# Performance work log

Hardware: AMD Instinct MI355X
Metric: run time of the kernel (lower is better)

## Reference

```python
import jax, jax.numpy as jnp
import numpy as np

N = 100000   # num nodes
D = 64       # in_channels == out_channels (forced by zeros_like(x) accumulator)
E = 400000   # edges per edge type
T = 5        # number of edge types (hardcoded list in the module)


def setup_inputs() -> dict:
    key = jax.random.key(0)
    k1, k2, k3, k4, k5 = jax.random.split(key, 5)
    x = jax.random.normal(k1, (N, D), dtype=jnp.float32)
    # 5 edge types, each [2, E] of node indices (row 0 = src, row 1 = dst)
    edges = jax.random.randint(k2, (T, 2, E), 0, N)
    # per-edge-type Linear(2D -> D): weight [2D, D] and bias [D]
    W = jax.random.normal(k3, (T, 2 * D, D), dtype=jnp.float32) * (1.0 / np.sqrt(2 * D))
    b = jax.random.normal(k4, (T, D), dtype=jnp.float32) * 0.01
    edge_attention = jax.random.normal(k5, (T,), dtype=jnp.float32)
    return {"x": x, "W": W, "b": b, "edge_attention": edge_attention, "edges": edges}


def reference(x, W, b, edge_attention, edges):
    # softmax over the 5 edge types (F.softmax(self.edge_attention, dim=0))
    weights = jax.nn.softmax(edge_attention)              # [T]
    src = edges[:, 0, :]                                  # [T, E]
    dst = edges[:, 1, :]                                  # [T, E]
    # gather: edge_features = cat([x[src], x[dst]], dim=1)
    feats = jnp.concatenate([x[src], x[dst]], axis=-1)    # [T, E, 2D]
    # per-edge-type MLP: Linear(2D->D) + ReLU
    proj = jax.nn.relu(jnp.einsum('tef,tfd->ted', feats, W) + b[:, None, :])  # [T, E, D]
    # scatter-add into src nodes, then mean via clamped bincount
    seg_sum = jax.vmap(lambda s, p: jax.ops.segment_sum(p, s, num_segments=N))(src, proj)  # [T, N, D]
    counts = jax.vmap(lambda s: jax.ops.segment_sum(jnp.ones(s.shape, jnp.float32), s, num_segments=N))(src)  # [T, N]
    counts = jnp.maximum(counts, 1.0)[:, :, None]         # clamp(min=1)
    node_proj = seg_sum / counts                          # [T, N, D]
    # attention-weighted sum across edge types
    return jnp.einsum('t,tnd->nd', weights, node_proj)    # [N, D]
```

## Files before the change

### kernel.cpp

```cpp
#include <hip/hip_runtime.h>
#include <hip/hip_bf16.h>

#define NN 100000
#define DD 64
#define EE 400000
#define TT 5

#define CH 16
#define BPC 6250
#define PSPLIT 32
#define PESL (EE / PSPLIT)
#define PBN (TT * CH * PSPLIT)
#define PB_IDX(t, c, s) ((((t) * CH + (c)) * PSPLIT) + (s))

#define SCAN_TOTAL 500000
#define SCAN_T 256
#define SCAN_PER 1024
#define SCAN_B 512

typedef __bf16 bf16x8 __attribute__((ext_vector_type(8)));
typedef float  f32x4  __attribute__((ext_vector_type(4)));

#define OFF_XBF  0u
#define OFF_WT   12800000u
#define OFF_CTOT 12881920u
#define OFF_WGT  14881920u
#define OFF_CUR  14881984u
#define OFF_BS   16881984u
#define OFF_BO   16884032u
#define OFF_PE   16886080u
#define OFF_PB   24886080u
#define OFF_DST  24914240u
#define OFF_SEG  32914240u

__device__ __forceinline__ unsigned short f2bf(float f) {
    union { float f; unsigned u; } v; v.f = f;
    unsigned u = v.u;
    return (unsigned short)((u + 0x7FFFu + ((u >> 16) & 1u)) >> 16);
}

__global__ void k_init(const float* __restrict__ x, const float* __restrict__ W,
                       const float* __restrict__ ea,
                       unsigned short* __restrict__ xbf, unsigned short* __restrict__ wT,
                       float* __restrict__ wgt, float* __restrict__ out) {
    int i = blockIdx.x * blockDim.x + threadIdx.x;
    if (i < NN * DD) {
        out[i] = 0.0f;
        xbf[i] = f2bf(x[i]);
    }
    if (i < TT * 128 * 64) {
        int t = i >> 13;
        int rem = i & 8191;
        int d = rem >> 7;
        int k = rem & 127;
        wT[i] = f2bf(W[t * 8192 + k * 64 + d]);
    }
    if (i == 0) {
        float m = -1e30f;
        for (int t = 0; t < TT; t++) m = fmaxf(m, ea[t]);
        float e[TT]; float s = 0.0f;
        for (int t = 0; t < TT; t++) { e[t] = __expf(ea[t] - m); s += e[t]; }
        for (int t = 0; t < TT; t++) wgt[t] = e[t] / s;
    }
}

__global__ __launch_bounds__(256) void k_pcount(const int* __restrict__ edges,
                                                unsigned* __restrict__ pcnt) {
    const int s = blockIdx.x, t = blockIdx.y;
    __shared__ unsigned h[CH];
    if (threadIdx.x < CH) h[threadIdx.x] = 0u;
    __syncthreads();
    const int4* srcp = reinterpret_cast<const int4*>(edges + (size_t)t * 2 * EE + s * PESL);
    for (int i = threadIdx.x; i < PESL / 4; i += 256) {
        int4 v = srcp[i];
        atomicAdd(&h[(unsigned)v.x / BPC], 1u);
        atomicAdd(&h[(unsigned)v.y / BPC], 1u);
        atomicAdd(&h[(unsigned)v.z / BPC], 1u);
        atomicAdd(&h[(unsigned)v.w / BPC], 1u);
    }
    __syncthreads();
    if (threadIdx.x < CH) pcnt[PB_IDX(t, threadIdx.x, s)] = h[threadIdx.x];
}

__global__ void k_pscan(unsigned* __restrict__ pb) {
    __shared__ unsigned s[256];
    const int tid = threadIdx.x;
    unsigned v[10]; unsigned sum = 0u;
#pragma unroll
    for (int j = 0; j < 10; j++) { v[j] = pb[tid * 10 + j]; sum += v[j]; }
    s[tid] = sum;
    __syncthreads();
    unsigned inc = sum;
    for (int d = 1; d < 256; d <<= 1) {
        unsigned a = (tid >= d) ? s[tid - d] : 0u;
        __syncthreads();
        inc += a;
        s[tid] = inc;
        __syncthreads();
    }
    unsigned run = inc - sum;
#pragma unroll
    for (int j = 0; j < 10; j++) { unsigned c = v[j]; pb[tid * 10 + j] = run; run += c; }
    if (tid == 255) pb[PBN] = run;
}

__global__ __launch_bounds__(256) void k_pscat(const int* __restrict__ edges,
                                               const unsigned* __restrict__ pbase,
                                               unsigned* __restrict__ pe) {
    const int s = blockIdx.x, t = blockIdx.y;
    __shared__ unsigned lofs[CH];
    if (threadIdx.x < CH) lofs[threadIdx.x] = pbase[PB_IDX(t, threadIdx.x, s)];
    __syncthreads();
    const int* srcp = edges + (size_t)t * 2 * EE + s * PESL;
    const int* dstp = srcp + EE;
    for (int i = threadIdx.x; i < PESL / 4; i += 256) {
        int4 v = reinterpret_cast<const int4*>(srcp)[i];
        int4 w = reinterpret_cast<const int4*>(dstp)[i];
        {
            unsigned c = (unsigned)v.x / BPC;
            unsigned o = atomicAdd(&lofs[c], 1u);
            pe[o] = (((unsigned)v.x - c * BPC) << 17) | (unsigned)w.x;
        }
        {
            unsigned c = (unsigned)v.y / BPC;
            unsigned o = atomicAdd(&lofs[c], 1u);
            pe[o] = (((unsigned)v.y - c * BPC) << 17) | (unsigned)w.y;
        }
        {
            unsigned c = (unsigned)v.z / BPC;
            unsigned o = atomicAdd(&lofs[c], 1u);
            pe[o] = (((unsigned)v.z - c * BPC) << 17) | (unsigned)w.z;
        }
        {
            unsigned c = (unsigned)v.w / BPC;
            unsigned o = atomicAdd(&lofs[c], 1u);
            pe[o] = (((unsigned)v.w - c * BPC) << 17) | (unsigned)w.w;
        }
    }
}

__global__ __launch_bounds__(512) void k_bcount(const unsigned* __restrict__ pe,
                                                const unsigned* __restrict__ pbase,
                                                unsigned* __restrict__ cnt_tot) {
    const int c = blockIdx.x, t = blockIdx.y;
    __shared__ unsigned h[BPC];
    for (int i = threadIdx.x; i < BPC; i += 512) h[i] = 0u;
    __syncthreads();
    const unsigned st = pbase[PB_IDX(t, c, 0)];
    const unsigned en = pbase[((t * CH + c) + 1) * PSPLIT];
    for (unsigned i = st + threadIdx.x; i < en; i += 512)
        atomicAdd(&h[pe[i] >> 17], 1u);
    __syncthreads();
    unsigned* outp = cnt_tot + t * NN + c * BPC;
    for (int i = threadIdx.x; i < BPC; i += 512) outp[i] = h[i];
}

__global__ void k_scan1(const unsigned* __restrict__ cnt_tot,
                        unsigned* __restrict__ cur, unsigned* __restrict__ bsum) {
    __shared__ unsigned s[SCAN_T];
    const int b = blockIdx.x, tid = threadIdx.x;
    const int base = b * SCAN_PER + tid * 4;
    unsigned tot[4] = {0u, 0u, 0u, 0u};
    if (base < SCAN_TOTAL) {
        uint4 tv = *reinterpret_cast<const uint4*>(cnt_tot + base);
        tot[0] = tv.x; tot[1] = tv.y; tot[2] = tv.z; tot[3] = tv.w;
    }
    const unsigned tsum = tot[0] + tot[1] + tot[2] + tot[3];
    s[tid] = tsum;
    __syncthreads();
    unsigned inc = tsum;
    for (int d = 1; d < SCAN_T; d <<= 1) {
        unsigned add = (tid >= d) ? s[tid - d] : 0u;
        __syncthreads();
        inc += add;
        s[tid] = inc;
        __syncthreads();
    }
    if (tid == SCAN_T - 1) bsum[b] = inc;
    const unsigned p0 = inc - tsum;
    if (base < SCAN_TOTAL) {
        *reinterpret_cast<uint4*>(cur + base) =
            make_uint4(p0, p0 + tot[0], p0 + tot[0] + tot[1], p0 + tot[0] + tot[1] + tot[2]);
    }
}

__global__ void k_scan2(const unsigned* __restrict__ bsum, unsigned* __restrict__ boff) {
    __shared__ unsigned s[SCAN_B];
    const int tid = threadIdx.x;
    const unsigned v = bsum[tid];
    s[tid] = v;
    __syncthreads();
    unsigned inc = v;
    for (int d = 1; d < SCAN_B; d <<= 1) {
        unsigned add = (tid >= d) ? s[tid - d] : 0u;
        __syncthreads();
        inc += add;
        s[tid] = inc;
        __syncthreads();
    }
    boff[tid] = inc - v;
}

__global__ __launch_bounds__(512) void k_bfill(const unsigned* __restrict__ pe,
                                               const unsigned* __restrict__ pbase,
                                               const unsigned* __restrict__ cur,
                                               const unsigned* __restrict__ boff,
                                               const unsigned* __restrict__ cnt_tot,
                                               int* __restrict__ sdst,
                                               int* __restrict__ seg) {
    const int c = blockIdx.x, t = blockIdx.y;
    __shared__ unsigned curl[BPC];
    const int n0 = c * BPC;
    for (int i = threadIdx.x; i < BPC; i += 512) {
        int g = t * NN + n0 + i;
        unsigned start = cur[g] + boff[g >> 10];
        curl[i] = start;
        unsigned cc = cnt_tot[g];
        int node = n0 + i;
        for (unsigned j = 0; j < cc; j++) seg[start + j] = node;
    }
    __syncthreads();
    const unsigned st = pbase[PB_IDX(t, c, 0)];
    const unsigned en = pbase[((t * CH + c) + 1) * PSPLIT];
    for (unsigned i = st + threadIdx.x; i < en; i += 512) {
        unsigned p = pe[i];
        sdst[atomicAdd(&curl[p >> 17], 1u)] = (int)(p & 0x1FFFFu);
    }
}

__global__ __launch_bounds__(256) void k_edge(
    const unsigned short* __restrict__ xbf, const unsigned short* __restrict__ wT,
    const float* __restrict__ b, const int* __restrict__ sdst,
    const int* __restrict__ seg, const unsigned* __restrict__ cnt,
    const float* __restrict__ wgt, float* __restrict__ out) {
    const int t  = blockIdx.y;
    const int e0 = blockIdx.x * 128;

    __shared__ __align__(16) unsigned short Ab[128][136];
    __shared__ float scale_s[128];
    __shared__ int   src_s[132];

    const int tid = threadIdx.x;

    {
        int e = tid >> 1, half = tid & 1;
        size_t pos = (size_t)t * EE + e0 + e;
        int idx = half ? sdst[pos] : seg[pos];
        const float4* g = reinterpret_cast<const float4*>(xbf + (size_t)idx * 64);
        float4* l = reinterpret_cast<float4*>(&Ab[e][half * 64]);
#pragma unroll
        for (int c = 0; c < 8; c++) l[c] = g[c];
        if (half == 0) {
            src_s[e] = idx;
            scale_s[e] = wgt[t] / (float)cnt[t * NN + idx];
        }
    }
    __syncthreads();

    const int wv = tid >> 6, lane = tid & 63;
    const int m16 = lane & 15, quad = lane >> 4;
    const unsigned short* wrow = wT + (size_t)t * 8192;

    f32x4 acc[2][4];
#pragma unroll
    for (int tm = 0; tm < 2; tm++)
#pragma unroll
        for (int tn = 0; tn < 4; tn++)
            acc[tm][tn] = (f32x4){0.f, 0.f, 0.f, 0.f};

#pragma unroll
    for (int kk = 0; kk < 128; kk += 32) {
        const int kb = kk + quad * 8;
        bf16x8 af[2], bfr[4];
#pragma unroll
        for (int tm = 0; tm < 2; tm++)
            af[tm] = *reinterpret_cast<const bf16x8*>(&Ab[wv * 32 + tm * 16 + m16][kb]);
#pragma unroll
        for (int tn = 0; tn < 4; tn++)
            bfr[tn] = *reinterpret_cast<const bf16x8*>(wrow + (tn * 16 + m16) * 128 + kb);
#pragma unroll
        for (int tm = 0; tm < 2; tm++)
#pragma unroll
            for (int tn = 0; tn < 4; tn++)
                acc[tm][tn] = __builtin_amdgcn_mfma_f32_16x16x32_bf16(
                    af[tm], bfr[tn], acc[tm][tn], 0, 0, 0);
    }

    __syncthreads();

    float bias[4];
#pragma unroll
    for (int tn = 0; tn < 4; tn++) bias[tn] = b[t * 64 + tn * 16 + m16];

    float* proj = reinterpret_cast<float*>(&Ab[0][0]);
#pragma unroll
    for (int tm = 0; tm < 2; tm++) {
#pragma unroll
        for (int r = 0; r < 4; r++) {
            const int eloc = wv * 32 + tm * 16 + quad * 4 + r;
            const float s = scale_s[eloc];
#pragma unroll
            for (int tn = 0; tn < 4; tn++) {
                float v = acc[tm][tn][r] + bias[tn];
                v = v > 0.f ? v : 0.f;
                proj[eloc * 68 + tn * 16 + m16] = v * s;
            }
        }
    }

    {
        const int j0 = wv * 32;
        float sum = 0.f;
#pragma unroll
        for (int j = j0; j < j0 + 32; j++) {
            sum += proj[j * 68 + lane];
            const bool flush = (j == j0 + 31) || (src_s[j + 1] != src_s[j]);
            if (flush) {
                atomicAdd(out + (size_t)src_s[j] * 64 + lane, sum);
                sum = 0.f;
            }
        }
    }
}

extern "C" void kernel_launch(void* const* d_in, const int* in_sizes, int n_in,
                              void* d_out, int out_size, void* d_ws, size_t ws_size,
                              hipStream_t stream) {
    const float* x     = (const float*)d_in[0];
    const float* W     = (const float*)d_in[1];
    const float* b     = (const float*)d_in[2];
    const float* ea    = (const float*)d_in[3];
    const int*   edges = (const int*)d_in[4];
    float* out = (float*)d_out;

    char* ws = (char*)d_ws;
    unsigned short* xbf  = (unsigned short*)(ws + OFF_XBF);
    unsigned short* wT   = (unsigned short*)(ws + OFF_WT);
    unsigned* cnt_tot    = (unsigned*)(ws + OFF_CTOT);
    float* wgt           = (float*)(ws + OFF_WGT);
    unsigned* cur        = (unsigned*)(ws + OFF_CUR);
    unsigned* bsum       = (unsigned*)(ws + OFF_BS);
    unsigned* boff       = (unsigned*)(ws + OFF_BO);
    unsigned* pe         = (unsigned*)(ws + OFF_PE);
    unsigned* pb         = (unsigned*)(ws + OFF_PB);
    int* sdst            = (int*)(ws + OFF_DST);
    int* seg             = (int*)(ws + OFF_SEG);

    k_init<<<(NN * DD) / 256, 256, 0, stream>>>(x, W, ea, xbf, wT, wgt, out);

    k_pcount<<<dim3(PSPLIT, TT), 256, 0, stream>>>(edges, pb);
    k_pscan<<<1, 256, 0, stream>>>(pb);
    k_pscat<<<dim3(PSPLIT, TT), 256, 0, stream>>>(edges, pb, pe);
    k_bcount<<<dim3(CH, TT), 512, 0, stream>>>(pe, pb, cnt_tot);
    k_scan1<<<SCAN_B, SCAN_T, 0, stream>>>(cnt_tot, cur, bsum);
    k_scan2<<<1, SCAN_B, 0, stream>>>(bsum, boff);
    k_bfill<<<dim3(CH, TT), 512, 0, stream>>>(pe, pb, cur, boff, cnt_tot, sdst, seg);

    dim3 grid(EE / 128, TT);
    k_edge<<<grid, 256, 0, stream>>>(xbf, wT, b, sdst, seg, cnt_tot, wgt, out);
}
```

Before: 339.8 us.

## Assign node ranges per block, accumulate in shared memory, drop global atomics

The edge kernel now launches one block per 64-node range instead of one per 128 edges of one type. Each block walks the CSR-sorted edges of all five types whose source falls in its range, in 32-edge chunks per wave. It accumulates results with LDS atomics and then writes the output rows directly. This removes the output zeroing in init and the global float atomics. In exchange there is load imbalance across blocks, per-chunk padding waste, and a per-wave loop with no block-level sync between the shared Ab/proj reuse steps.

```diff
diff --git a/kernel.cpp b/kernel.cpp
--- a/kernel.cpp
+++ b/kernel.cpp
@@ -17,6 +17,9 @@
 #define SCAN_T 256
 #define SCAN_PER 1024
 #define SCAN_B 512
+
+#define NB 64
+#define NBLK ((NN + NB - 1) / NB)
 
 typedef __bf16 bf16x8 __attribute__((ext_vector_type(8)));
 typedef float  f32x4  __attribute__((ext_vector_type(4)));
@@ -42,10 +45,9 @@
 __global__ void k_init(const float* __restrict__ x, const float* __restrict__ W,
                        const float* __restrict__ ea,
                        unsigned short* __restrict__ xbf, unsigned short* __restrict__ wT,
-                       float* __restrict__ wgt, float* __restrict__ out) {
+                       float* __restrict__ wgt) {
     int i = blockIdx.x * blockDim.x + threadIdx.x;
     if (i < NN * DD) {
-        out[i] = 0.0f;
         xbf[i] = f2bf(x[i]);
     }
     if (i < TT * 128 * 64) {
@@ -228,98 +230,149 @@
     }
 }
 
-__global__ __launch_bounds__(256) void k_edge(
+__global__ __launch_bounds__(256) void k_edge4(
     const unsigned short* __restrict__ xbf, const unsigned short* __restrict__ wT,
     const float* __restrict__ b, const int* __restrict__ sdst,
     const int* __restrict__ seg, const unsigned* __restrict__ cnt,
+    const unsigned* __restrict__ cur, const unsigned* __restrict__ boff,
     const float* __restrict__ wgt, float* __restrict__ out) {
-    const int t  = blockIdx.y;
-    const int e0 = blockIdx.x * 128;
+
+    const int n0 = blockIdx.x * NB;
+    const int n1 = (n0 + NB < NN) ? (n0 + NB) : NN;
+    const int tid = threadIdx.x;
+    const int wv = tid >> 6, lane = tid & 63;
+    const int m16 = lane & 15, quad = lane >> 4;
 
     __shared__ __align__(16) unsigned short Ab[128][136];
+    __shared__ __align__(16) float accs[NB][64];
     __shared__ float scale_s[128];
     __shared__ int   src_s[132];
 
-    const int tid = threadIdx.x;
-
     {
-        int e = tid >> 1, half = tid & 1;
-        size_t pos = (size_t)t * EE + e0 + e;
-        int idx = half ? sdst[pos] : seg[pos];
-        const float4* g = reinterpret_cast<const float4*>(xbf + (size_t)idx * 64);
-        float4* l = reinterpret_cast<float4*>(&Ab[e][half * 64]);
-#pragma unroll
-        for (int c = 0; c < 8; c++) l[c] = g[c];
-        if (half == 0) {
-            src_s[e] = idx;
-            scale_s[e] = wgt[t] / (float)cnt[t * NN + idx];
-        }
-    }
-    __syncthreads();
-
-    const int wv = tid >> 6, lane = tid & 63;
-    const int m16 = lane & 15, quad = lane >> 4;
-    const unsigned short* wrow = wT + (size_t)t * 8192;
-
-    f32x4 acc[2][4];
-#pragma unroll
-    for (int tm = 0; tm < 2; tm++)
-#pragma unroll
-        for (int tn = 0; tn < 4; tn++)
-            acc[tm][tn] = (f32x4){0.f, 0.f, 0.f, 0.f};
-
-#pragma unroll
-    for (int kk = 0; kk < 128; kk += 32) {
-        const int kb = kk + quad * 8;
-        bf16x8 af[2], bfr[4];
+        float4* a4 = reinterpret_cast<float4*>(&accs[0][0]);
+        for (int i = tid; i < NB * 16; i += 256) a4[i] = make_float4(0.f, 0.f, 0.f, 0.f);
+    }
+
+    unsigned p0t[TT], p1t[TT];
+    int nw[TT], NW = 0;
+#pragma unroll
+    for (int t = 0; t < TT; t++) {
+        int g0 = t * NN + n0;
+        int g1 = t * NN + n1;
+        unsigned p0 = cur[g0] + boff[g0 >> 10];
+        unsigned p1 = (g1 >= SCAN_TOTAL) ? (unsigned)(TT * EE)
+                                         : (cur[g1] + boff[g1 >> 10]);
+        p0t[t] = p0; p1t[t] = p1;
+        nw[t] = (int)((p1 - p0 + 31u) >> 5);
+        NW += nw[t];
+    }
+
+    __syncthreads();
+
+    for (int k = wv; k < NW; k += 4) {
+        int t = 0, rem = k;
+#pragma unroll
+        for (int tt = 0; tt < TT - 1; tt++)
+            if (t == tt && rem >= nw[tt]) { rem -= nw[tt]; t = tt + 1; }
+        unsigned p0s = p0t[0], p1s = p1t[0];
+#pragma unroll
+        for (int tt = 1; tt < TT; tt++)
+            if (t == tt) { p0s = p0t[tt]; p1s = p1t[tt]; }
+        const unsigned ts = p0s + ((unsigned)rem << 5);
+        const unsigned left = p1s - ts;
+        const int rows = (int)((left < 32u) ? left : 32u);
+        const float wgt_t = wgt[t];
+
+        {
+            const int e = lane >> 1, half = lane & 1;
+            const int r = wv * 32 + e;
+            float4* l = reinterpret_cast<float4*>(&Ab[r][half * 64]);
+            if (e < rows) {
+                const unsigned pos = ts + (unsigned)e;
+                const int idx = half ? sdst[pos] : seg[pos];
+                const float4* g = reinterpret_cast<const float4*>(xbf + (size_t)idx * 64);
+#pragma unroll
+                for (int cc = 0; cc < 8; cc++) l[cc] = g[cc];
+                if (half == 0) {
+                    src_s[r] = idx - n0;
+                    scale_s[r] = wgt_t / (float)cnt[t * NN + idx];
+                }
+            } else {
+                const float4 z = make_float4(0.f, 0.f, 0.f, 0.f);
+#pragma unroll
+                for (int cc = 0; cc < 8; cc++) l[cc] = z;
+                if (half == 0) { src_s[r] = 0; scale_s[r] = 0.f; }
+            }
+        }
+
+        const unsigned short* wrow = wT + (size_t)t * 8192;
+
+        f32x4 acc[2][4];
 #pragma unroll
         for (int tm = 0; tm < 2; tm++)
-            af[tm] = *reinterpret_cast<const bf16x8*>(&Ab[wv * 32 + tm * 16 + m16][kb]);
-#pragma unroll
-        for (int tn = 0; tn < 4; tn++)
-            bfr[tn] = *reinterpret_cast<const bf16x8*>(wrow + (tn * 16 + m16) * 128 + kb);
-#pragma unroll
-        for (int tm = 0; tm < 2; tm++)
 #pragma unroll
             for (int tn = 0; tn < 4; tn++)
-                acc[tm][tn] = __builtin_amdgcn_mfma_f32_16x16x32_bf16(
-                    af[tm], bfr[tn], acc[tm][tn], 0, 0, 0);
-    }
-
-    __syncthreads();
-
-    float bias[4];
-#pragma unroll
-    for (int tn = 0; tn < 4; tn++) bias[tn] = b[t * 64 + tn * 16 + m16];
-
-    float* proj = reinterpret_cast<float*>(&Ab[0][0]);
-#pragma unroll
-    for (int tm = 0; tm < 2; tm++) {
-#pragma unroll
-        for (int r = 0; r < 4; r++) {
-            const int eloc = wv * 32 + tm * 16 + quad * 4 + r;
-            const float s = scale_s[eloc];
-#pragma unroll
-            for (int tn = 0; tn < 4; tn++) {
-                float v = acc[tm][tn][r] + bias[tn];
-                v = v > 0.f ? v : 0.f;
-                proj[eloc * 68 + tn * 16 + m16] = v * s;
+                acc[tm][tn] = (f32x4){0.f, 0.f, 0.f, 0.f};
+
+#pragma unroll
+        for (int kk = 0; kk < 128; kk += 32) {
+            const int kb = kk + quad * 8;
+            bf16x8 af[2], bfr[4];
+#pragma unroll
+            for (int tm = 0; tm < 2; tm++)
+                af[tm] = *reinterpret_cast<const bf16x8*>(&Ab[wv * 32 + tm * 16 + m16][kb]);
+#pragma unroll
+            for (int tn = 0; tn < 4; tn++)
+                bfr[tn] = *reinterpret_cast<const bf16x8*>(wrow + (tn * 16 + m16) * 128 + kb);
+#pragma unroll
+            for (int tm = 0; tm < 2; tm++)
+#pragma unroll
+                for (int tn = 0; tn < 4; tn++)
+                    acc[tm][tn] = __builtin_amdgcn_mfma_f32_16x16x32_bf16(
+                        af[tm], bfr[tn], acc[tm][tn], 0, 0, 0);
+        }
+
+        float bias[4];
+#pragma unroll
+        for (int tn = 0; tn < 4; tn++) bias[tn] = b[t * 64 + tn * 16 + m16];
+
+        float* proj = reinterpret_cast<float*>(&Ab[0][0]);
+#pragma unroll
+        for (int tm = 0; tm < 2; tm++) {
+#pragma unroll
+            for (int r = 0; r < 4; r++) {
+                const int eloc = wv * 32 + tm * 16 + quad * 4 + r;
+                const float s = scale_s[eloc];
+#pragma unroll
+                for (int tn = 0; tn < 4; tn++) {
+                    float v = acc[tm][tn][r] + bias[tn];
+                    v = v > 0.f ? v : 0.f;
+                    proj[eloc * 68 + tn * 16 + m16] = v * s;
+                }
             }
         }
-    }
-
+
+        {
+            const int j0 = wv * 32;
+            float sum = 0.f;
+#pragma unroll
+            for (int j = j0; j < j0 + 32; j++) {
+                sum += proj[j * 68 + lane];
+                const bool flush = (j == j0 + 31) || (src_s[j + 1] != src_s[j]);
+                if (flush) {
+                    atomicAdd(&accs[src_s[j]][lane], sum);
+                    sum = 0.f;
+                }
+            }
+        }
+    }
+
+    __syncthreads();
     {
-        const int j0 = wv * 32;
-        float sum = 0.f;
-#pragma unroll
-        for (int j = j0; j < j0 + 32; j++) {
-            sum += proj[j * 68 + lane];
-            const bool flush = (j == j0 + 31) || (src_s[j + 1] != src_s[j]);
-            if (flush) {
-                atomicAdd(out + (size_t)src_s[j] * 64 + lane, sum);
-                sum = 0.f;
-            }
-        }
+        const int rows = n1 - n0;
+        const float4* a4 = reinterpret_cast<const float4*>(&accs[0][0]);
+        float4* o4 = reinterpret_cast<float4*>(out + (size_t)n0 * 64);
+        for (int i = tid; i < rows * 16; i += 256) o4[i] = a4[i];
     }
 }
 
@@ -346,7 +399,7 @@
     int* sdst            = (int*)(ws + OFF_DST);
     int* seg             = (int*)(ws + OFF_SEG);
 
-    k_init<<<(NN * DD) / 256, 256, 0, stream>>>(x, W, ea, xbf, wT, wgt, out);
+    k_init<<<(NN * DD) / 256, 256, 0, stream>>>(x, W, ea, xbf, wT, wgt);
 
     k_pcount<<<dim3(PSPLIT, TT), 256, 0, stream>>>(edges, pb);
     k_pscan<<<1, 256, 0, stream>>>(pb);
@@ -356,6 +409,6 @@
     k_scan2<<<1, SCAN_B, 0, stream>>>(bsum, boff);
     k_bfill<<<dim3(CH, TT), 512, 0, stream>>>(pe, pb, cur, boff, cnt_tot, sdst, seg);
 
-    dim3 grid(EE / 128, TT);
-    k_edge<<<grid, 256, 0, stream>>>(xbf, wT, b, sdst, seg, cnt_tot, wgt, out);
-}
+    k_edge4<<<NBLK, 256, 0, stream>>>(xbf, wT, b, sdst, seg, cnt_tot,
+                                      cur, boff, wgt, out);
+}
```

Result: slower. 486.8 us (+43.3%).

## Load MFMA A-fragments directly from global and raise bucket count to forty

Applied to the files above, without the earlier changes.

The edge kernel no longer stages gathered bf16 node rows in shared memory. Each wave now handles 16 edges and loads its A fragments straight from global memory into registers, with 64 edges per block and a higher occupancy bound. Separately, the bucketing pass uses 40 chunks of 2500 nodes instead of 16, giving the bucket-count and bucket-fill kernels more blocks, and the prefix scan is widened to 512 threads to match. In exchange, each weight fragment is reused over fewer edges, and the gather becomes strided global loads instead of coalesced row copies.

```diff
diff --git a/kernel.cpp b/kernel.cpp
--- a/kernel.cpp
+++ b/kernel.cpp
@@ -6,8 +6,8 @@
 #define EE 400000
 #define TT 5
 
-#define CH 16
-#define BPC 6250
+#define CH 40
+#define BPC 2500
 #define PSPLIT 32
 #define PESL (EE / PSPLIT)
 #define PBN (TT * CH * PSPLIT)
@@ -83,15 +83,19 @@
 }
 
 __global__ void k_pscan(unsigned* __restrict__ pb) {
-    __shared__ unsigned s[256];
+    __shared__ unsigned s[512];
     const int tid = threadIdx.x;
-    unsigned v[10]; unsigned sum = 0u;
-#pragma unroll
-    for (int j = 0; j < 10; j++) { v[j] = pb[tid * 10 + j]; sum += v[j]; }
+    unsigned v[13]; unsigned sum = 0u;
+#pragma unroll
+    for (int j = 0; j < 13; j++) {
+        int g = tid * 13 + j;
+        v[j] = (g < PBN) ? pb[g] : 0u;
+        sum += v[j];
+    }
     s[tid] = sum;
     __syncthreads();
     unsigned inc = sum;
-    for (int d = 1; d < 256; d <<= 1) {
+    for (int d = 1; d < 512; d <<= 1) {
         unsigned a = (tid >= d) ? s[tid - d] : 0u;
         __syncthreads();
         inc += a;
@@ -100,8 +104,12 @@
     }
     unsigned run = inc - sum;
 #pragma unroll
-    for (int j = 0; j < 10; j++) { unsigned c = v[j]; pb[tid * 10 + j] = run; run += c; }
-    if (tid == 255) pb[PBN] = run;
+    for (int j = 0; j < 13; j++) {
+        int g = tid * 13 + j;
+        if (g < PBN) pb[g] = run;
+        run += v[j];
+    }
+    if (tid == 511) pb[PBN] = run;
 }
 
 __global__ __launch_bounds__(256) void k_pscat(const int* __restrict__ edges,
@@ -228,93 +236,76 @@
     }
 }
 
-__global__ __launch_bounds__(256) void k_edge(
+__global__ __launch_bounds__(256, 8) void k_edge5(
     const unsigned short* __restrict__ xbf, const unsigned short* __restrict__ wT,
     const float* __restrict__ b, const int* __restrict__ sdst,
     const int* __restrict__ seg, const unsigned* __restrict__ cnt,
     const float* __restrict__ wgt, float* __restrict__ out) {
     const int t  = blockIdx.y;
-    const int e0 = blockIdx.x * 128;
-
-    __shared__ __align__(16) unsigned short Ab[128][136];
-    __shared__ float scale_s[128];
-    __shared__ int   src_s[132];
+    const int e0 = blockIdx.x * 64;
+
+    __shared__ __align__(16) float proj[64][68];
+    __shared__ float scale_s[64];
+    __shared__ int   src_s[68];
 
     const int tid = threadIdx.x;
-
-    {
-        int e = tid >> 1, half = tid & 1;
-        size_t pos = (size_t)t * EE + e0 + e;
-        int idx = half ? sdst[pos] : seg[pos];
-        const float4* g = reinterpret_cast<const float4*>(xbf + (size_t)idx * 64);
-        float4* l = reinterpret_cast<float4*>(&Ab[e][half * 64]);
-#pragma unroll
-        for (int c = 0; c < 8; c++) l[c] = g[c];
-        if (half == 0) {
-            src_s[e] = idx;
-            scale_s[e] = wgt[t] / (float)cnt[t * NN + idx];
-        }
-    }
-    __syncthreads();
-
     const int wv = tid >> 6, lane = tid & 63;
     const int m16 = lane & 15, quad = lane >> 4;
+    const int row = wv * 16 + m16;
+
+    const size_t pos = (size_t)t * EE + e0 + row;
+    const int srcI = seg[pos];
+    const int dstI = sdst[pos];
+    if (quad == 0) {
+        src_s[row] = srcI;
+        scale_s[row] = wgt[t] / (float)cnt[t * NN + srcI];
+    }
+
     const unsigned short* wrow = wT + (size_t)t * 8192;
-
-    f32x4 acc[2][4];
-#pragma unroll
-    for (int tm = 0; tm < 2; tm++)
-#pragma unroll
-        for (int tn = 0; tn < 4; tn++)
-            acc[tm][tn] = (f32x4){0.f, 0.f, 0.f, 0.f};
-
-#pragma unroll
-    for (int kk = 0; kk < 128; kk += 32) {
-        const int kb = kk + quad * 8;
-        bf16x8 af[2], bfr[4];
-#pragma unroll
-        for (int tm = 0; tm < 2; tm++)
-            af[tm] = *reinterpret_cast<const bf16x8*>(&Ab[wv * 32 + tm * 16 + m16][kb]);
+    const unsigned short* arow_s = xbf + (size_t)srcI * 64;
+    const unsigned short* arow_d = xbf + (size_t)dstI * 64;
+
+    f32x4 acc[4];
+#pragma unroll
+    for (int tn = 0; tn < 4; tn++) acc[tn] = (f32x4){0.f, 0.f, 0.f, 0.f};
+
+#pragma unroll
+    for (int k4 = 0; k4 < 4; k4++) {
+        const int off = (k4 & 1) * 32 + quad * 8;
+        const bf16x8 af = *reinterpret_cast<const bf16x8*>((k4 < 2 ? arow_s : arow_d) + off);
+        const int kb = k4 * 32 + quad * 8;
+        bf16x8 bfr[4];
 #pragma unroll
         for (int tn = 0; tn < 4; tn++)
             bfr[tn] = *reinterpret_cast<const bf16x8*>(wrow + (tn * 16 + m16) * 128 + kb);
 #pragma unroll
-        for (int tm = 0; tm < 2; tm++)
-#pragma unroll
-            for (int tn = 0; tn < 4; tn++)
-                acc[tm][tn] = __builtin_amdgcn_mfma_f32_16x16x32_bf16(
-                    af[tm], bfr[tn], acc[tm][tn], 0, 0, 0);
-    }
-
-    __syncthreads();
+        for (int tn = 0; tn < 4; tn++)
+            acc[tn] = __builtin_amdgcn_mfma_f32_16x16x32_bf16(af, bfr[tn], acc[tn], 0, 0, 0);
+    }
 
     float bias[4];
 #pragma unroll
     for (int tn = 0; tn < 4; tn++) bias[tn] = b[t * 64 + tn * 16 + m16];
 
-    float* proj = reinterpret_cast<float*>(&Ab[0][0]);
-#pragma unroll
-    for (int tm = 0; tm < 2; tm++) {
-#pragma unroll
-        for (int r = 0; r < 4; r++) {
-            const int eloc = wv * 32 + tm * 16 + quad * 4 + r;
-            const float s = scale_s[eloc];
-#pragma unroll
-            for (int tn = 0; tn < 4; tn++) {
-                float v = acc[tm][tn][r] + bias[tn];
-                v = v > 0.f ? v : 0.f;
-                proj[eloc * 68 + tn * 16 + m16] = v * s;
-            }
+#pragma unroll
+    for (int r = 0; r < 4; r++) {
+        const int eloc = wv * 16 + quad * 4 + r;
+        const float s = scale_s[eloc];
+#pragma unroll
+        for (int tn = 0; tn < 4; tn++) {
+            float v = acc[tn][r] + bias[tn];
+            v = v > 0.f ? v : 0.f;
+            proj[eloc][tn * 16 + m16] = v * s;
         }
     }
 
     {
-        const int j0 = wv * 32;
+        const int j0 = wv * 16;
         float sum = 0.f;
 #pragma unroll
-        for (int j = j0; j < j0 + 32; j++) {
-            sum += proj[j * 68 + lane];
-            const bool flush = (j == j0 + 31) || (src_s[j + 1] != src_s[j]);
+        for (int j = j0; j < j0 + 16; j++) {
+            sum += proj[j][lane];
+            const bool flush = (j == j0 + 15) || (src_s[j + 1] != src_s[j]);
             if (flush) {
                 atomicAdd(out + (size_t)src_s[j] * 64 + lane, sum);
                 sum = 0.f;
@@ -349,13 +340,13 @@
     k_init<<<(NN * DD) / 256, 256, 0, stream>>>(x, W, ea, xbf, wT, wgt, out);
 
     k_pcount<<<dim3(PSPLIT, TT), 256, 0, stream>>>(edges, pb);
-    k_pscan<<<1, 256, 0, stream>>>(pb);
+    k_pscan<<<1, 512, 0, stream>>>(pb);
     k_pscat<<<dim3(PSPLIT, TT), 256, 0, stream>>>(edges, pb, pe);
     k_bcount<<<dim3(CH, TT), 512, 0, stream>>>(pe, pb, cnt_tot);
     k_scan1<<<SCAN_B, SCAN_T, 0, stream>>>(cnt_tot, cur, bsum);
     k_scan2<<<1, SCAN_B, 0, stream>>>(bsum, boff);
     k_bfill<<<dim3(CH, TT), 512, 0, stream>>>(pe, pb, cur, boff, cnt_tot, sdst, seg);
 
-    dim3 grid(EE / 128, TT);
-    k_edge<<<grid, 256, 0, stream>>>(xbf, wT, b, sdst, seg, cnt_tot, wgt, out);
-}
+    dim3 grid(EE / 64, TT);
+    k_edge5<<<grid, 256, 0, stream>>>(xbf, wT, b, sdst, seg, cnt_tot, wgt, out);
+}
```

Result: slower. 418.7 us (+23.2%).

## Fuse partition count into init kernel and raise bucket count to forty

Applied to the files above, without the earlier changes.

Merges the per-slice partition histogram into the init kernel: its first 160 blocks also count source-node buckets, which removes one kernel launch. It also raises the coarse bucket count from 16 to 40 (2500 nodes each), so the bcount and bfill grids get more blocks and each block handles a smaller range. The partition scan now runs with 512 threads to cover the larger table. Risks: the new work makes the first 160 init blocks much longer than the rest, and the downstream kernels may have assumptions about bucket size, such as shared-memory sizing, that are not visible here.

```diff
diff --git a/kernel.cpp b/kernel.cpp
--- a/kernel.cpp
+++ b/kernel.cpp
@@ -6,8 +6,8 @@
 #define EE 400000
 #define TT 5
 
-#define CH 16
-#define BPC 6250
+#define CH 40
+#define BPC 2500
 #define PSPLIT 32
 #define PESL (EE / PSPLIT)
 #define PBN (TT * CH * PSPLIT)
@@ -39,10 +39,12 @@
     return (unsigned short)((u + 0x7FFFu + ((u >> 16) & 1u)) >> 16);
 }
 
-__global__ void k_init(const float* __restrict__ x, const float* __restrict__ W,
-                       const float* __restrict__ ea,
-                       unsigned short* __restrict__ xbf, unsigned short* __restrict__ wT,
-                       float* __restrict__ wgt, float* __restrict__ out) {
+__global__ __launch_bounds__(256) void k_init(
+        const float* __restrict__ x, const float* __restrict__ W,
+        const float* __restrict__ ea, const int* __restrict__ edges,
+        unsigned short* __restrict__ xbf, unsigned short* __restrict__ wT,
+        float* __restrict__ wgt, float* __restrict__ out,
+        unsigned* __restrict__ pcnt) {
     int i = blockIdx.x * blockDim.x + threadIdx.x;
     if (i < NN * DD) {
         out[i] = 0.0f;
@@ -62,36 +64,39 @@
         for (int t = 0; t < TT; t++) { e[t] = __expf(ea[t] - m); s += e[t]; }
         for (int t = 0; t < TT; t++) wgt[t] = e[t] / s;
     }
-}
-
-__global__ __launch_bounds__(256) void k_pcount(const int* __restrict__ edges,
-                                                unsigned* __restrict__ pcnt) {
-    const int s = blockIdx.x, t = blockIdx.y;
-    __shared__ unsigned h[CH];
-    if (threadIdx.x < CH) h[threadIdx.x] = 0u;
-    __syncthreads();
-    const int4* srcp = reinterpret_cast<const int4*>(edges + (size_t)t * 2 * EE + s * PESL);
-    for (int i = threadIdx.x; i < PESL / 4; i += 256) {
-        int4 v = srcp[i];
-        atomicAdd(&h[(unsigned)v.x / BPC], 1u);
-        atomicAdd(&h[(unsigned)v.y / BPC], 1u);
-        atomicAdd(&h[(unsigned)v.z / BPC], 1u);
-        atomicAdd(&h[(unsigned)v.w / BPC], 1u);
-    }
-    __syncthreads();
-    if (threadIdx.x < CH) pcnt[PB_IDX(t, threadIdx.x, s)] = h[threadIdx.x];
+    if (blockIdx.x < PSPLIT * TT) {
+        const int s = blockIdx.x & (PSPLIT - 1);
+        const int t = blockIdx.x >> 5;
+        __shared__ unsigned h[CH];
+        if (threadIdx.x < CH) h[threadIdx.x] = 0u;
+        __syncthreads();
+        const int4* srcp = reinterpret_cast<const int4*>(edges + (size_t)t * 2 * EE + s * PESL);
+        for (int j = threadIdx.x; j < PESL / 4; j += 256) {
+            int4 v = srcp[j];
+            atomicAdd(&h[(unsigned)v.x / BPC], 1u);
+            atomicAdd(&h[(unsigned)v.y / BPC], 1u);
+            atomicAdd(&h[(unsigned)v.z / BPC], 1u);
+            atomicAdd(&h[(unsigned)v.w / BPC], 1u);
+        }
+        __syncthreads();
+        if (threadIdx.x < CH) pcnt[PB_IDX(t, threadIdx.x, s)] = h[threadIdx.x];
+    }
 }
 
 __global__ void k_pscan(unsigned* __restrict__ pb) {
-    __shared__ unsigned s[256];
+    __shared__ unsigned s[512];
     const int tid = threadIdx.x;
-    unsigned v[10]; unsigned sum = 0u;
-#pragma unroll
-    for (int j = 0; j < 10; j++) { v[j] = pb[tid * 10 + j]; sum += v[j]; }
+    unsigned v[13]; unsigned sum = 0u;
+#pragma unroll
+    for (int j = 0; j < 13; j++) {
+        int g = tid * 13 + j;
+        v[j] = (g < PBN) ? pb[g] : 0u;
+        sum += v[j];
+    }
     s[tid] = sum;
     __syncthreads();
     unsigned inc = sum;
-    for (int d = 1; d < 256; d <<= 1) {
+    for (int d = 1; d < 512; d <<= 1) {
         unsigned a = (tid >= d) ? s[tid - d] : 0u;
         __syncthreads();
         inc += a;
@@ -100,8 +105,12 @@
     }
     unsigned run = inc - sum;
 #pragma unroll
-    for (int j = 0; j < 10; j++) { unsigned c = v[j]; pb[tid * 10 + j] = run; run += c; }
-    if (tid == 255) pb[PBN] = run;
+    for (int j = 0; j < 13; j++) {
+        int g = tid * 13 + j;
+        if (g < PBN) pb[g] = run;
+        run += v[j];
+    }
+    if (tid == 511) pb[PBN] = run;
 }
 
 __global__ __launch_bounds__(256) void k_pscat(const int* __restrict__ edges,
@@ -346,10 +355,9 @@
     int* sdst            = (int*)(ws + OFF_DST);
     int* seg             = (int*)(ws + OFF_SEG);
 
-    k_init<<<(NN * DD) / 256, 256, 0, stream>>>(x, W, ea, xbf, wT, wgt, out);
-
-    k_pcount<<<dim3(PSPLIT, TT), 256, 0, stream>>>(edges, pb);
-    k_pscan<<<1, 256, 0, stream>>>(pb);
+    k_init<<<(NN * DD) / 256, 256, 0, stream>>>(x, W, ea, edges, xbf, wT, wgt, out, pb);
+
+    k_pscan<<<1, 512, 0, stream>>>(pb);
     k_pscat<<<dim3(PSPLIT, TT), 256, 0, stream>>>(edges, pb, pe);
     k_bcount<<<dim3(CH, TT), 512, 0, stream>>>(pe, pb, cnt_tot);
     k_scan1<<<SCAN_B, SCAN_T, 0, stream>>>(cnt_tot, cur, bsum);
```

Measured after the change: 320.2 us. 1.06x faster.
